# Kernel tuning notes

Hardware: AMD Instinct MI355X
Metric: run time of the kernel (lower is better)

Reference implementation:

```python
import jax, jax.numpy as jnp
import numpy as np

N, SD, VD, LD = 8192, 512, 4096, 768
TAU = 0.5
K = 6    # topk over stru->mm similarity
K2 = 6   # topk2 over mm->mm similarity
BN_EPS = 1e-5
LRELU_SLOPE = 0.01


def _mlp_bn(x, W1, b1, W2, b2, gamma, beta):
    # Linear -> LeakyReLU -> Linear -> BatchNorm1d (training mode, batch stats)
    h = x @ W1 + b1
    h = jnp.where(h >= 0, h, LRELU_SLOPE * h)
    h = h @ W2 + b2
    mu = h.mean(axis=0)
    var = h.var(axis=0)  # biased variance, as torch BN uses for normalization
    return (h - mu) / jnp.sqrt(var + BN_EPS) * gamma + beta


def _cossim(x, y):
    xn = x / (jnp.linalg.norm(x, axis=-1, keepdims=True) + 1e-12)
    yn = y / (jnp.linalg.norm(y, axis=-1, keepdims=True) + 1e-12)
    return xn @ yn.T


def _neibor_mnce_v2(stru, mm):
    sm = jnp.exp(_cossim(stru, mm) / TAU)   # [N, N]
    mmd = _cossim(mm, mm)                    # [N, N]
    _, maxSM = jax.lax.top_k(sm, K)          # [N, K]
    rows = jnp.arange(stru.shape[0])[:, None]
    pos = []
    for i in range(K):  # fixed small loop over topk columns (as in original)
        idx = maxSM[:, i]                         # [N]
        _, mm_idx = jax.lax.top_k(mmd[idx], K2)   # gather rows then topk -> [N, K2]
        pos.append(sm[rows, mm_idx])              # [N, K2]
    pos = jnp.concatenate(pos, axis=-1)           # [N, K*K2]
    return jnp.mean(-jnp.log(pos.sum(-1) / sm.sum(-1)))


def setup_inputs() -> dict:
    key = jax.random.key(0)
    ks = jax.random.split(key, 11)
    d = {
        'stru_feats': jax.random.normal(ks[0], (N, SD), jnp.float32),
        'visu_feats': jax.random.normal(ks[1], (N, VD), jnp.float32),
        'ling_feats': jax.random.normal(ks[2], (N, LD), jnp.float32),
        # fusion_l_vl params
        'Wl1': jax.random.normal(ks[3], (LD, SD), jnp.float32) / np.sqrt(LD),
        'bl1': jnp.zeros((SD,), jnp.float32),
        'Wl2': jax.random.normal(ks[4], (SD, SD), jnp.float32) / np.sqrt(SD),
        'bl2': jnp.zeros((SD,), jnp.float32),
        'gl': jnp.ones((SD,), jnp.float32),
        'betal': jnp.zeros((SD,), jnp.float32),
        # fusion_v_vl params
        'Wv1': jax.random.normal(ks[5], (VD, SD), jnp.float32) / np.sqrt(VD),
        'bv1': jnp.zeros((SD,), jnp.float32),
        'Wv2': jax.random.normal(ks[6], (SD, SD), jnp.float32) / np.sqrt(SD),
        'bv2': jnp.zeros((SD,), jnp.float32),
        'gv': jnp.ones((SD,), jnp.float32),
        'betav': jnp.zeros((SD,), jnp.float32),
    }
    return d


def reference(stru_feats, visu_feats, ling_feats,
              Wl1, bl1, Wl2, bl2, gl, betal,
              Wv1, bv1, Wv2, bv2, gv, betav):
    ling = _mlp_bn(ling_feats, Wl1, bl1, Wl2, bl2, gl, betal)
    visu = _mlp_bn(visu_feats, Wv1, bv1, Wv2, bv2, gv, betav)
    loss_sl = _neibor_mnce_v2(stru_feats, ling)
    loss_sv = _neibor_mnce_v2(stru_feats, visu)
    return (loss_sl + loss_sv, ling, visu)
```

## Files before the change

### kernel.cpp

```cpp
#include <hip/hip_runtime.h>
#include <hip/hip_bf16.h>
#include <math.h>

typedef __bf16 bf16;
typedef __attribute__((ext_vector_type(8))) __bf16 bf16x8;
typedef __attribute__((ext_vector_type(4))) float floatx4;

static_assert(sizeof(bf16x8) == 16, "bf16x8 must be 16B");

__global__ void row_normalize_kernel(const float* __restrict__ x, bf16* __restrict__ out) {
  __shared__ float red[256];
  int row = blockIdx.x;
  int t = threadIdx.x;
  float v0 = x[(size_t)row * 512 + t];
  float v1 = x[(size_t)row * 512 + t + 256];
  red[t] = v0 * v0 + v1 * v1;
  __syncthreads();
  for (int d = 128; d > 0; d >>= 1) {
    if (t < d) red[t] += red[t + d];
    __syncthreads();
  }
  float scale = 1.0f / (sqrtf(red[0]) + 1e-12f);
  out[(size_t)row * 512 + t] = (bf16)(v0 * scale);
  out[(size_t)row * 512 + t + 256] = (bf16)(v1 * scale);
}

__global__ void transpose_cast_kernel(const float* __restrict__ W, bf16* __restrict__ Wt, int K) {
  __shared__ float t[64][65];
  int k0 = blockIdx.x * 64;
  int n0 = blockIdx.y * 64;
#pragma unroll
  for (int m = 0; m < 16; ++m) {
    int kk = (threadIdx.x >> 6) + m * 4;
    int nn = threadIdx.x & 63;
    t[kk][nn] = W[(size_t)(k0 + kk) * 512 + n0 + nn];
  }
  __syncthreads();
#pragma unroll
  for (int m = 0; m < 16; ++m) {
    int nn = (threadIdx.x >> 6) + m * 4;
    int kk = threadIdx.x & 63;
    Wt[(size_t)(n0 + nn) * K + k0 + kk] = (bf16)t[kk][nn];
  }
}

__global__ void bn_stats_kernel(const float* __restrict__ h, float* __restrict__ colsum,
                                float* __restrict__ colsumsq) {
  int col = threadIdx.x;
  int r0 = blockIdx.x * 32;
  float s = 0.f, s2 = 0.f;
  for (int r = r0; r < r0 + 32; ++r) {
    float v = h[(size_t)r * 512 + col];
    s += v;
    s2 += v * v;
  }
  atomicAdd(&colsum[col], s);
  atomicAdd(&colsumsq[col], s2);
}

__global__ void bn_apply_kernel(const float* __restrict__ h, const float* __restrict__ colsum,
                                const float* __restrict__ colsumsq, const float* __restrict__ gamma,
                                const float* __restrict__ beta, float* __restrict__ mm_out,
                                bf16* __restrict__ mmn) {
  __shared__ float red[512];
  int row = blockIdx.x, col = threadIdx.x;
  float mean = colsum[col] * (1.0f / 8192.0f);
  float var = colsumsq[col] * (1.0f / 8192.0f) - mean * mean;
  float inv = rsqrtf(var + 1e-5f);
  float y = (h[(size_t)row * 512 + col] - mean) * inv * gamma[col] + beta[col];
  mm_out[(size_t)row * 512 + col] = y;
  red[col] = y * y;
  __syncthreads();
  for (int d = 256; d > 0; d >>= 1) {
    if (col < d) red[col] += red[col + d];
    __syncthreads();
  }
  float scale = 1.0f / (sqrtf(red[0]) + 1e-12f);
  mmn[(size_t)row * 512 + col] = (bf16)(y * scale);
}

template <int MODE, bool AF32>
__launch_bounds__(256, 2) __global__
void gemm_nt_kernel(const void* __restrict__ Av, const bf16* __restrict__ B,
                    const float* __restrict__ bias, bf16* __restrict__ out_bf,
                    float* __restrict__ out_f, int K) {
  __shared__ __align__(16) bf16 As[2][128][64];
  __shared__ __align__(16) bf16 Bs[2][64][64];

  const int tid = threadIdx.x;
  const int lane = tid & 63;
  const int wave = tid >> 6;
  const int q = lane >> 4;
  const int ml = lane & 15;
  const int row0 = blockIdx.x * 128;
  const int col0 = blockIdx.y * 64;

  const float* Af = (const float*)Av;
  const bf16* Ab = (const bf16*)Av;

  const int sr = tid >> 3;
  const int sc = tid & 7;

  floatx4 acc[2][4];
#pragma unroll
  for (int g = 0; g < 2; ++g)
#pragma unroll
    for (int f = 0; f < 4; ++f) acc[g][f] = (floatx4)0.0f;

  {
#pragma unroll
    for (int m = 0; m < 4; ++m) {
      int r = sr + m * 32;
      bf16x8 v;
      if constexpr (AF32) {
        const float* p = Af + (size_t)(row0 + r) * K + sc * 8;
#pragma unroll
        for (int e = 0; e < 8; ++e) v[e] = (bf16)p[e];
      } else {
        v = *(const bf16x8*)(Ab + (size_t)(row0 + r) * K + sc * 8);
      }
      *(bf16x8*)&As[0][r][(sc ^ (r & 7)) * 8] = v;
    }
#pragma unroll
    for (int m = 0; m < 2; ++m) {
      int r = sr + m * 32;
      *(bf16x8*)&Bs[0][r][(sc ^ (r & 7)) * 8] =
          *(const bf16x8*)(B + (size_t)(col0 + r) * K + sc * 8);
    }
  }

  const int nsteps = K >> 6;
  int buf = 0;
  for (int s = 0; s < nsteps; ++s) {
    __syncthreads();
    const bool has_next = (s + 1) < nsteps;
    floatx4 af[4][2];
    bf16x8 ab[4];
    bf16x8 bb[2];
    if (has_next) {
      const int kt = (s + 1) << 6;
#pragma unroll
      for (int m = 0; m < 4; ++m) {
        if constexpr (AF32) {
          const floatx4* p = (const floatx4*)(Af + (size_t)(row0 + sr + m * 32) * K + kt + sc * 8);
          af[m][0] = p[0];
          af[m][1] = p[1];
        } else {
          ab[m] = *(const bf16x8*)(Ab + (size_t)(row0 + sr + m * 32) * K + kt + sc * 8);
        }
      }
#pragma unroll
      for (int m = 0; m < 2; ++m)
        bb[m] = *(const bf16x8*)(B + (size_t)(col0 + sr + m * 32) * K + kt + sc * 8);
    }
#pragma unroll
    for (int kh = 0; kh < 2; ++kh) {
      const int slot = ((q + kh * 4) ^ (ml & 7)) * 8;
      bf16x8 a0 = *(const bf16x8*)&As[buf][wave * 32 + ml][slot];
      bf16x8 a1 = *(const bf16x8*)&As[buf][wave * 32 + 16 + ml][slot];
#pragma unroll
      for (int f = 0; f < 4; ++f) {
        bf16x8 b = *(const bf16x8*)&Bs[buf][f * 16 + ml][slot];
        acc[0][f] = __builtin_amdgcn_mfma_f32_16x16x32_bf16(a0, b, acc[0][f], 0, 0, 0);
        acc[1][f] = __builtin_amdgcn_mfma_f32_16x16x32_bf16(a1, b, acc[1][f], 0, 0, 0);
      }
    }
    if (has_next) {
#pragma unroll
      for (int m = 0; m < 4; ++m) {
        int r = sr + m * 32;
        bf16x8 v;
        if constexpr (AF32) {
#pragma unroll
          for (int e = 0; e < 8; ++e) v[e] = (bf16)af[m][e >> 2][e & 3];
        } else {
          v = ab[m];
        }
        *(bf16x8*)&As[buf ^ 1][r][(sc ^ (r & 7)) * 8] = v;
      }
#pragma unroll
      for (int m = 0; m < 2; ++m) {
        int r = sr + m * 32;
        *(bf16x8*)&Bs[buf ^ 1][r][(sc ^ (r & 7)) * 8] = bb[m];
      }
    }
    buf ^= 1;
  }

#pragma unroll
  for (int f = 0; f < 4; ++f) {
    int colg = col0 + f * 16 + ml;
    float bv = bias[colg];
#pragma unroll
    for (int g = 0; g < 2; ++g)
#pragma unroll
      for (int i = 0; i < 4; ++i) {
        int rowg = row0 + wave * 32 + g * 16 + q * 4 + i;
        float v = acc[g][f][i] + bv;
        if constexpr (MODE == 0) {
          v = v >= 0.f ? v : 0.01f * v;
          out_bf[(size_t)rowg * 512 + colg] = (bf16)v;
        } else {
          out_f[(size_t)rowg * 512 + colg] = v;
        }
      }
  }
}

__device__ __forceinline__ unsigned pack_key(float v, int col) {
  unsigned u = __float_as_uint(v);
  u = (u & 0x80000000u) ? ~u : (u | 0x80000000u);
  return (u & 0xFFFFE000u) | (unsigned)(8191 - col);
}

#define NPARTS 16

template <bool DO_SM>
__launch_bounds__(256, 2) __global__
void topk_sm_kernel(const bf16* __restrict__ A, const bf16* __restrict__ B,
                    unsigned* __restrict__ part_keys, float* __restrict__ rowsum_part) {
  __shared__ __align__(16) bf16 Bs[2][64][128];

  const int tid = threadIdx.x;
  const int lane = tid & 63;
  const int wave = tid >> 6;
  const int q = lane >> 4;
  const int ml = lane & 15;
  const int row0 = blockIdx.x * 128;
  const int part = blockIdx.y;

  const int str = tid >> 4;
  const int scu = tid & 15;
  const int ssc = scu ^ str;

  bf16x8 afr[2][16];
#pragma unroll
  for (int g = 0; g < 2; ++g) {
    const bf16* ap = A + (size_t)(row0 + wave * 32 + g * 16 + ml) * 512 + q * 8;
#pragma unroll
    for (int s = 0; s < 16; ++s) afr[g][s] = *(const bf16x8*)(ap + s * 32);
  }

  unsigned p6[2][4][6];
#pragma unroll
  for (int g = 0; g < 2; ++g)
#pragma unroll
    for (int i = 0; i < 4; ++i)
#pragma unroll
      for (int j = 0; j < 6; ++j) p6[g][i][j] = 0u;
  float srow[2][4] = {{0.f, 0.f, 0.f, 0.f}, {0.f, 0.f, 0.f, 0.f}};

  int buf = 0;
  {
    const bf16* bp = B + (size_t)(part * 512 + str) * 512 + scu * 8;
#pragma unroll
    for (int m = 0; m < 4; ++m)
      *(bf16x8*)&Bs[0][str + m * 16][ssc * 8] = *(const bf16x8*)(bp + (size_t)m * 16 * 512);
  }

  for (int ct = 0; ct < 8; ++ct) {
    const int col0 = part * 512 + ct * 64;
    floatx4 acc[2][4];
#pragma unroll
    for (int g = 0; g < 2; ++g)
#pragma unroll
      for (int f = 0; f < 4; ++f) acc[g][f] = (floatx4)0.0f;

#pragma unroll
    for (int kt4 = 0; kt4 < 4; ++kt4) {
      __syncthreads();
      bf16x8 st[4];
      const bool has_next = !(ct == 7 && kt4 == 3);
      if (has_next) {
        const int nct = (kt4 == 3) ? ct + 1 : ct;
        const int nk = (kt4 == 3) ? 0 : (kt4 + 1) * 128;
        const bf16* bp = B + (size_t)(part * 512 + nct * 64 + str) * 512 + nk + scu * 8;
#pragma unroll
        for (int m = 0; m < 4; ++m) st[m] = *(const bf16x8*)(bp + (size_t)m * 16 * 512);
      }
#pragma unroll
      for (int kk2 = 0; kk2 < 4; ++kk2) {
#pragma unroll
        for (int f = 0; f < 4; ++f) {
          const int sc2 = (kk2 * 4 + q) ^ ml;
          bf16x8 b = *(const bf16x8*)&Bs[buf][f * 16 + ml][sc2 * 8];
          acc[0][f] = __builtin_amdgcn_mfma_f32_16x16x32_bf16(afr[0][kt4 * 4 + kk2], b, acc[0][f], 0, 0, 0);
          acc[1][f] = __builtin_amdgcn_mfma_f32_16x16x32_bf16(afr[1][kt4 * 4 + kk2], b, acc[1][f], 0, 0, 0);
        }
      }
      if (has_next) {
#pragma unroll
        for (int m = 0; m < 4; ++m)
          *(bf16x8*)&Bs[buf ^ 1][str + m * 16][ssc * 8] = st[m];
      }
      buf ^= 1;
    }

#pragma unroll
    for (int g = 0; g < 2; ++g)
#pragma unroll
      for (int i = 0; i < 4; ++i) {
        if constexpr (DO_SM) {
          float s = 0.f;
#pragma unroll
          for (int f = 0; f < 4; ++f) s += __expf(2.0f * acc[g][f][i]);
          srow[g][i] += s;
        }
#pragma unroll
        for (int f = 0; f < 4; ++f) {
          unsigned key = pack_key(acc[g][f][i], col0 + f * 16 + ml);
          if (key > p6[g][i][5]) {
#pragma unroll
            for (int j = 5; j >= 1; --j) {
              bool ap = key > p6[g][i][j - 1];
              unsigned keep = (key > p6[g][i][j]) ? key : p6[g][i][j];
              p6[g][i][j] = ap ? p6[g][i][j - 1] : keep;
            }
            if (key > p6[g][i][0]) p6[g][i][0] = key;
          }
        }
      }
  }

#pragma unroll
  for (int g = 0; g < 2; ++g)
#pragma unroll
    for (int i = 0; i < 4; ++i) {
      const int lrow = wave * 32 + g * 16 + q * 4 + i;
      if constexpr (DO_SM) {
        float s = srow[g][i];
        s += __shfl_xor(s, 1);
        s += __shfl_xor(s, 2);
        s += __shfl_xor(s, 4);
        s += __shfl_xor(s, 8);
        if (ml == 0) rowsum_part[(size_t)(row0 + lrow) * NPARTS + part] = s;
      }
      const size_t o = ((size_t)(row0 + lrow) * NPARTS + part) * 6;
#pragma unroll
      for (int k = 0; k < 6; ++k) {
        unsigned mk = p6[g][i][0];
#pragma unroll
        for (int d = 1; d < 16; d <<= 1) {
          unsigned ok = (unsigned)__shfl_xor((int)mk, d);
          if (ok > mk) mk = ok;
        }
        if (ml == 0) part_keys[o + k] = mk;
        if (p6[g][i][0] == mk) {
#pragma unroll
          for (int j = 0; j < 5; ++j) p6[g][i][j] = p6[g][i][j + 1];
          p6[g][i][5] = 0u;
        }
      }
    }
}

__global__ void merge_top6_kernel(const unsigned* __restrict__ part_keys,
                                  int* __restrict__ out_idx,
                                  const float* __restrict__ rowsum_part, float* __restrict__ rowsum,
                                  int do_rowsum) {
  int row = blockIdx.x * blockDim.x + threadIdx.x;
  if (row >= 8192) return;
  unsigned best[6] = {0u, 0u, 0u, 0u, 0u, 0u};
  for (int p = 0; p < NPARTS; ++p) {
#pragma unroll
    for (int c = 0; c < 6; ++c) {
      unsigned k = part_keys[((size_t)row * NPARTS + p) * 6 + c];
      if (k > best[5]) {
#pragma unroll
        for (int j = 5; j >= 1; --j) {
          bool ap = k > best[j - 1];
          unsigned keep = (k > best[j]) ? k : best[j];
          best[j] = ap ? best[j - 1] : keep;
        }
        if (k > best[0]) best[0] = k;
      }
    }
  }
#pragma unroll
  for (int j = 0; j < 6; ++j) out_idx[row * 6 + j] = 8191 - (int)(best[j] & 0x1FFFu);
  if (do_rowsum) {
    float s = 0.f;
    for (int p = 0; p < NPARTS; ++p) s += rowsum_part[(size_t)row * NPARTS + p];
    rowsum[row] = s;
  }
}

__global__ void loss_kernel(const bf16* __restrict__ strun, const bf16* __restrict__ mmn,
                            const int* __restrict__ top6, const int* __restrict__ nbr,
                            const float* __restrict__ rowsum, float* __restrict__ out0) {
  int w = (int)((blockIdx.x * blockDim.x + threadIdx.x) >> 6);
  int lane = threadIdx.x & 63;
  if (w >= 8192) return;
  bf16x8 sv = *(const bf16x8*)(strun + (size_t)w * 512 + lane * 8);
  float sf[8];
#pragma unroll
  for (int e = 0; e < 8; ++e) sf[e] = (float)sv[e];
  float pos = 0.f;
  for (int k = 0; k < 6; ++k) {
    int j = top6[w * 6 + k];
#pragma unroll
    for (int l = 0; l < 6; ++l) {
      int m = nbr[j * 6 + l];
      bf16x8 mv = *(const bf16x8*)(mmn + (size_t)m * 512 + lane * 8);
      float d = 0.f;
#pragma unroll
      for (int e = 0; e < 8; ++e) d += sf[e] * (float)mv[e];
      d += __shfl_xor(d, 1);
      d += __shfl_xor(d, 2);
      d += __shfl_xor(d, 4);
      d += __shfl_xor(d, 8);
      d += __shfl_xor(d, 16);
      d += __shfl_xor(d, 32);
      pos += __expf(2.0f * d);
    }
  }
  if (lane == 0) {
    float loss_r = logf(rowsum[w]) - logf(pos);
    atomicAdd(out0, loss_r * (1.0f / 8192.0f));
  }
}

extern "C" void kernel_launch(void* const* d_in, const int* in_sizes, int n_in, void* d_out,
                              int out_size, void* d_ws, size_t ws_size, hipStream_t stream) {
  const float* stru = (const float*)d_in[0];
  const float* visu = (const float*)d_in[1];
  const float* ling = (const float*)d_in[2];
  const float* Wl1 = (const float*)d_in[3];
  const float* bl1 = (const float*)d_in[4];
  const float* Wl2 = (const float*)d_in[5];
  const float* bl2 = (const float*)d_in[6];
  const float* gl = (const float*)d_in[7];
  const float* betal = (const float*)d_in[8];
  const float* Wv1 = (const float*)d_in[9];
  const float* bv1 = (const float*)d_in[10];
  const float* Wv2 = (const float*)d_in[11];
  const float* bv2 = (const float*)d_in[12];
  const float* gv = (const float*)d_in[13];
  const float* betav = (const float*)d_in[14];
  float* out = (float*)d_out;

  char* p = (char*)d_ws;
  auto alloc = [&](size_t bytes) {
    char* r = p;
    p += (bytes + 255) & ~(size_t)255;
    return r;
  };
  bf16* strun = (bf16*)alloc((size_t)8192 * 512 * 2);
  bf16* W1t = (bf16*)alloc((size_t)512 * 4096 * 2);
  bf16* W2t = (bf16*)alloc((size_t)512 * 512 * 2);
  bf16* H1 = (bf16*)alloc((size_t)8192 * 512 * 2);
  float* H2 = (float*)alloc((size_t)8192 * 512 * 4);
  bf16* mmn = (bf16*)alloc((size_t)8192 * 512 * 2);
  float* colsum = (float*)alloc(512 * 4);
  float* colsumsq = (float*)alloc(512 * 4);
  float* rowsum_part = (float*)alloc((size_t)8192 * NPARTS * 4);
  float* rowsum = (float*)alloc((size_t)8192 * 4);
  unsigned* part_keys = (unsigned*)alloc((size_t)8192 * NPARTS * 6 * 4);
  int* nbr = (int*)alloc((size_t)8192 * 6 * 4);
  int* top6 = (int*)alloc((size_t)8192 * 6 * 4);

  hipMemsetAsync(d_out, 0, 4, stream);
  row_normalize_kernel<<<8192, 256, 0, stream>>>(stru, strun);

  for (int br = 0; br < 2; ++br) {
    const float* X = (br == 0) ? ling : visu;
    int Kin = (br == 0) ? 768 : 4096;
    const float* W1 = (br == 0) ? Wl1 : Wv1;
    const float* b1 = (br == 0) ? bl1 : bv1;
    const float* W2 = (br == 0) ? Wl2 : Wv2;
    const float* b2 = (br == 0) ? bl2 : bv2;
    const float* g = (br == 0) ? gl : gv;
    const float* bet = (br == 0) ? betal : betav;
    float* mm_out = out + 1 + (size_t)br * 8192 * 512;

    transpose_cast_kernel<<<dim3(Kin / 64, 8), 256, 0, stream>>>(W1, W1t, Kin);
    transpose_cast_kernel<<<dim3(8, 8), 256, 0, stream>>>(W2, W2t, 512);

    gemm_nt_kernel<0, true><<<dim3(64, 8), 256, 0, stream>>>(
        X, W1t, b1, H1, nullptr, Kin);
    gemm_nt_kernel<1, false><<<dim3(64, 8), 256, 0, stream>>>(
        H1, W2t, b2, nullptr, H2, 512);

    hipMemsetAsync(colsum, 0, 512 * 4, stream);
    hipMemsetAsync(colsumsq, 0, 512 * 4, stream);
    bn_stats_kernel<<<256, 512, 0, stream>>>(H2, colsum, colsumsq);
    bn_apply_kernel<<<8192, 512, 0, stream>>>(H2, colsum, colsumsq, g, bet, mm_out, mmn);

    topk_sm_kernel<false><<<dim3(64, NPARTS), 256, 0, stream>>>(
        mmn, mmn, part_keys, nullptr);
    merge_top6_kernel<<<32, 256, 0, stream>>>(part_keys, nbr, nullptr, nullptr, 0);

    topk_sm_kernel<true><<<dim3(64, NPARTS), 256, 0, stream>>>(
        strun, mmn, part_keys, rowsum_part);
    merge_top6_kernel<<<32, 256, 0, stream>>>(part_keys, top6, rowsum_part, rowsum, 1);

    loss_kernel<<<2048, 256, 0, stream>>>(strun, mmn, top6, nbr, rowsum, out);
  }
}
```

Baseline: 1.202 ms.

## Fuse mm-mm and stru-mm topk passes sharing B tiles; precast X to bf16

Merges the two similarity/top-k kernels into one that computes mm·mm and stru·mm together for each 64-row block, so every loaded B tile in shared memory feeds both products and B is streamed once instead of twice. The grid changes to 128×8 with 1024 columns per part, keeping each block's MFMA work the same. Separately, when workspace allows, the first-layer input is cast to bf16 in its own kernel so the GEMM reads bf16 instead of converting fp32 on the fly. This adds an extra pass over the 8192×4096 input and a larger workspace requirement.

After: 1.116 ms. -7.2%, faster.

```diff
diff --git a/kernel.cpp b/kernel.cpp
--- a/kernel.cpp
+++ b/kernel.cpp
@@ -23,6 +23,21 @@
   float scale = 1.0f / (sqrtf(red[0]) + 1e-12f);
   out[(size_t)row * 512 + t] = (bf16)(v0 * scale);
   out[(size_t)row * 512 + t + 256] = (bf16)(v1 * scale);
+}
+
+__global__ void cast_bf16_kernel(const float* __restrict__ x, bf16* __restrict__ out, long n) {
+  long i = ((long)blockIdx.x * blockDim.x + threadIdx.x) * 8;
+  long stride = (long)gridDim.x * blockDim.x * 8;
+  for (; i < n; i += stride) {
+    floatx4 a = *(const floatx4*)(x + i);
+    floatx4 b = *(const floatx4*)(x + i + 4);
+    bf16x8 v;
+#pragma unroll
+    for (int e = 0; e < 4; ++e) v[e] = (bf16)a[e];
+#pragma unroll
+    for (int e = 0; e < 4; ++e) v[e + 4] = (bf16)b[e];
+    *(bf16x8*)(out + i) = v;
+  }
 }
 
 __global__ void transpose_cast_kernel(const float* __restrict__ W, bf16* __restrict__ Wt, int K) {
@@ -213,12 +228,12 @@
   return (u & 0xFFFFE000u) | (unsigned)(8191 - col);
 }
 
-#define NPARTS 16
-
-template <bool DO_SM>
+#define NPARTS 8
+
 __launch_bounds__(256, 2) __global__
-void topk_sm_kernel(const bf16* __restrict__ A, const bf16* __restrict__ B,
-                    unsigned* __restrict__ part_keys, float* __restrict__ rowsum_part) {
+void topk_sm_fused_kernel(const bf16* __restrict__ Amm, const bf16* __restrict__ Ast,
+                          const bf16* __restrict__ B, unsigned* __restrict__ keys_mm,
+                          unsigned* __restrict__ keys_sm, float* __restrict__ rowsum_part) {
   __shared__ __align__(16) bf16 Bs[2][64][128];
 
   const int tid = threadIdx.x;
@@ -226,7 +241,7 @@
   const int wave = tid >> 6;
   const int q = lane >> 4;
   const int ml = lane & 15;
-  const int row0 = blockIdx.x * 128;
+  const int row0 = blockIdx.x * 64;
   const int part = blockIdx.y;
 
   const int str = tid >> 4;
@@ -236,7 +251,7 @@
   bf16x8 afr[2][16];
 #pragma unroll
   for (int g = 0; g < 2; ++g) {
-    const bf16* ap = A + (size_t)(row0 + wave * 32 + g * 16 + ml) * 512 + q * 8;
+    const bf16* ap = (g == 0 ? Amm : Ast) + (size_t)(row0 + wave * 16 + ml) * 512 + q * 8;
 #pragma unroll
     for (int s = 0; s < 16; ++s) afr[g][s] = *(const bf16x8*)(ap + s * 32);
   }
@@ -248,18 +263,18 @@
     for (int i = 0; i < 4; ++i)
 #pragma unroll
       for (int j = 0; j < 6; ++j) p6[g][i][j] = 0u;
-  float srow[2][4] = {{0.f, 0.f, 0.f, 0.f}, {0.f, 0.f, 0.f, 0.f}};
+  float srow[4] = {0.f, 0.f, 0.f, 0.f};
 
   int buf = 0;
   {
-    const bf16* bp = B + (size_t)(part * 512 + str) * 512 + scu * 8;
+    const bf16* bp = B + (size_t)(part * 1024 + str) * 512 + scu * 8;
 #pragma unroll
     for (int m = 0; m < 4; ++m)
       *(bf16x8*)&Bs[0][str + m * 16][ssc * 8] = *(const bf16x8*)(bp + (size_t)m * 16 * 512);
   }
 
-  for (int ct = 0; ct < 8; ++ct) {
-    const int col0 = part * 512 + ct * 64;
+  for (int ct = 0; ct < 16; ++ct) {
+    const int col0 = part * 1024 + ct * 64;
     floatx4 acc[2][4];
 #pragma unroll
     for (int g = 0; g < 2; ++g)
@@ -270,11 +285,11 @@
     for (int kt4 = 0; kt4 < 4; ++kt4) {
       __syncthreads();
       bf16x8 st[4];
-      const bool has_next = !(ct == 7 && kt4 == 3);
+      const bool has_next = !(ct == 15 && kt4 == 3);
       if (has_next) {
         const int nct = (kt4 == 3) ? ct + 1 : ct;
         const int nk = (kt4 == 3) ? 0 : (kt4 + 1) * 128;
-        const bf16* bp = B + (size_t)(part * 512 + nct * 64 + str) * 512 + nk + scu * 8;
+        const bf16* bp = B + (size_t)(part * 1024 + nct * 64 + str) * 512 + nk + scu * 8;
 #pragma unroll
         for (int m = 0; m < 4; ++m) st[m] = *(const bf16x8*)(bp + (size_t)m * 16 * 512);
       }
@@ -297,15 +312,13 @@
     }
 
 #pragma unroll
-    for (int g = 0; g < 2; ++g)
-#pragma unroll
-      for (int i = 0; i < 4; ++i) {
-        if constexpr (DO_SM) {
-          float s = 0.f;
-#pragma unroll
-          for (int f = 0; f < 4; ++f) s += __expf(2.0f * acc[g][f][i]);
-          srow[g][i] += s;
-        }
+    for (int i = 0; i < 4; ++i) {
+      float s = 0.f;
+#pragma unroll
+      for (int f = 0; f < 4; ++f) s += __expf(2.0f * acc[1][f][i]);
+      srow[i] += s;
+#pragma unroll
+      for (int g = 0; g < 2; ++g)
 #pragma unroll
         for (int f = 0; f < 4; ++f) {
           unsigned key = pack_key(acc[g][f][i], col0 + f * 16 + ml);
@@ -319,22 +332,23 @@
             if (key > p6[g][i][0]) p6[g][i][0] = key;
           }
         }
-      }
-  }
-
-#pragma unroll
-  for (int g = 0; g < 2; ++g)
-#pragma unroll
-    for (int i = 0; i < 4; ++i) {
-      const int lrow = wave * 32 + g * 16 + q * 4 + i;
-      if constexpr (DO_SM) {
-        float s = srow[g][i];
-        s += __shfl_xor(s, 1);
-        s += __shfl_xor(s, 2);
-        s += __shfl_xor(s, 4);
-        s += __shfl_xor(s, 8);
-        if (ml == 0) rowsum_part[(size_t)(row0 + lrow) * NPARTS + part] = s;
-      }
+    }
+  }
+
+#pragma unroll
+  for (int i = 0; i < 4; ++i) {
+    const int lrow = wave * 16 + q * 4 + i;
+    {
+      float s = srow[i];
+      s += __shfl_xor(s, 1);
+      s += __shfl_xor(s, 2);
+      s += __shfl_xor(s, 4);
+      s += __shfl_xor(s, 8);
+      if (ml == 0) rowsum_part[(size_t)(row0 + lrow) * NPARTS + part] = s;
+    }
+#pragma unroll
+    for (int g = 0; g < 2; ++g) {
+      unsigned* dk = g ? keys_sm : keys_mm;
       const size_t o = ((size_t)(row0 + lrow) * NPARTS + part) * 6;
 #pragma unroll
       for (int k = 0; k < 6; ++k) {
@@ -344,7 +358,7 @@
           unsigned ok = (unsigned)__shfl_xor((int)mk, d);
           if (ok > mk) mk = ok;
         }
-        if (ml == 0) part_keys[o + k] = mk;
+        if (ml == 0) dk[o + k] = mk;
         if (p6[g][i][0] == mk) {
 #pragma unroll
           for (int j = 0; j < 5; ++j) p6[g][i][j] = p6[g][i][j + 1];
@@ -352,6 +366,7 @@
         }
       }
     }
+  }
 }
 
 __global__ void merge_top6_kernel(const unsigned* __restrict__ part_keys,
@@ -455,9 +470,15 @@
   float* colsumsq = (float*)alloc(512 * 4);
   float* rowsum_part = (float*)alloc((size_t)8192 * NPARTS * 4);
   float* rowsum = (float*)alloc((size_t)8192 * 4);
-  unsigned* part_keys = (unsigned*)alloc((size_t)8192 * NPARTS * 6 * 4);
+  unsigned* keys_mm = (unsigned*)alloc((size_t)8192 * NPARTS * 6 * 4);
+  unsigned* keys_sm = (unsigned*)alloc((size_t)8192 * NPARTS * 6 * 4);
   int* nbr = (int*)alloc((size_t)8192 * 6 * 4);
   int* top6 = (int*)alloc((size_t)8192 * 6 * 4);
+
+  size_t xb_bytes = (size_t)8192 * 4096 * 2;
+  size_t used = (size_t)(p - (char*)d_ws);
+  bf16* Xb = nullptr;
+  if (used + xb_bytes <= ws_size) Xb = (bf16*)alloc(xb_bytes);
 
   hipMemsetAsync(d_out, 0, 4, stream);
   row_normalize_kernel<<<8192, 256, 0, stream>>>(stru, strun);
@@ -476,8 +497,14 @@
     transpose_cast_kernel<<<dim3(Kin / 64, 8), 256, 0, stream>>>(W1, W1t, Kin);
     transpose_cast_kernel<<<dim3(8, 8), 256, 0, stream>>>(W2, W2t, 512);
 
-    gemm_nt_kernel<0, true><<<dim3(64, 8), 256, 0, stream>>>(
-        X, W1t, b1, H1, nullptr, Kin);
+    if (Xb) {
+      cast_bf16_kernel<<<2048, 256, 0, stream>>>(X, Xb, (long)8192 * Kin);
+      gemm_nt_kernel<0, false><<<dim3(64, 8), 256, 0, stream>>>(
+          Xb, W1t, b1, H1, nullptr, Kin);
+    } else {
+      gemm_nt_kernel<0, true><<<dim3(64, 8), 256, 0, stream>>>(
+          X, W1t, b1, H1, nullptr, Kin);
+    }
     gemm_nt_kernel<1, false><<<dim3(64, 8), 256, 0, stream>>>(
         H1, W2t, b2, nullptr, H2, 512);
 
@@ -486,13 +513,10 @@
     bn_stats_kernel<<<256, 512, 0, stream>>>(H2, colsum, colsumsq);
     bn_apply_kernel<<<8192, 512, 0, stream>>>(H2, colsum, colsumsq, g, bet, mm_out, mmn);
 
-    topk_sm_kernel<false><<<dim3(64, NPARTS), 256, 0, stream>>>(
-        mmn, mmn, part_keys, nullptr);
-    merge_top6_kernel<<<32, 256, 0, stream>>>(part_keys, nbr, nullptr, nullptr, 0);
-
-    topk_sm_kernel<true><<<dim3(64, NPARTS), 256, 0, stream>>>(
-        strun, mmn, part_keys, rowsum_part);
-    merge_top6_kernel<<<32, 256, 0, stream>>>(part_keys, top6, rowsum_part, rowsum, 1);
+    topk_sm_fused_kernel<<<dim3(128, NPARTS), 256, 0, stream>>>(
+        mmn, strun, mmn, keys_mm, keys_sm, rowsum_part);
+    merge_top6_kernel<<<32, 256, 0, stream>>>(keys_mm, nbr, nullptr, nullptr, 0);
+    merge_top6_kernel<<<32, 256, 0, stream>>>(keys_sm, top6, rowsum_part, rowsum, 1);
 
     loss_kernel<<<2048, 256, 0, stream>>>(strun, mmn, top6, nbr, rowsum, out);
   }
```
